# Kernel tuning notes

Measured on AMD Instinct MI355X. Metric: run time of the kernel, lower is better.

The kernel has to match this reference:

```python
import jax, jax.numpy as jnp
import numpy as np

NA_CUTOFF = 30.0
OTHER_CUTOFF = 15.0
THRESHOLDS = jnp.array([0.5, 1.0, 2.0, 4.0], dtype=jnp.float32)


def _cdist(x):
    # x: [b, n, 3] -> [b, n, n] euclidean distances, safe-sqrt (0 grad at 0)
    diff = x[:, :, None, :] - x[:, None, :, :]
    sq = jnp.sum(diff * diff, axis=-1)
    safe = jnp.where(sq > 0, sq, 1.0)
    return jnp.where(sq > 0, jnp.sqrt(safe), 0.0)


def setup_inputs() -> dict:
    key = jax.random.key(0)
    k1, k2, k3, k4, k5 = jax.random.split(key, 5)
    b, n = 2, 4096
    # angstrom-scale coordinates so cutoffs (15/30 A) are meaningful
    true_coords = jax.random.normal(k1, (b, n, 3), dtype=jnp.float32) * 20.0
    pred_coords = true_coords + jax.random.normal(k2, (b, n, 3), dtype=jnp.float32) * 1.0
    is_dna = jax.random.randint(k3, (b, n), 0, 2) > 0
    is_rna = jax.random.randint(k4, (b, n), 0, 2) > 0
    coords_mask = jax.random.randint(k5, (b, n), 0, 2) > 0
    return {
        'pred_coords': pred_coords,
        'true_coords': true_coords,
        'is_dna': is_dna,
        'is_rna': is_rna,
        'coords_mask': coords_mask,
    }


def reference(pred_coords, true_coords, is_dna, is_rna, coords_mask):
    b, n, _ = pred_coords.shape
    pred_dists = _cdist(pred_coords)            # [b, n, n]
    true_dists = _cdist(true_coords)            # [b, n, n]
    dist_diff = jnp.abs(true_dists - pred_dists)
    # eps: sigmoid(threshold - |d_true - d_pred|), averaged over 4 thresholds
    eps = jax.nn.sigmoid(THRESHOLDS - dist_diff[..., None]).mean(axis=-1)  # [b, n, n]

    is_nt = is_dna | is_rna
    nt_pair = is_nt[:, :, None] & is_nt[:, None, :]
    inclusion = jnp.where(nt_pair, true_dists < NA_CUTOFF, true_dists < OTHER_CUTOFF)
    mask = inclusion & ~jnp.eye(n, dtype=bool)[None]
    mask = mask & (coords_mask[:, :, None] & coords_mask[:, None, :])

    maskf = mask.astype(eps.dtype)
    num = (eps * maskf).sum(axis=(-1, -2))
    den = jnp.maximum(maskf.sum(axis=(-1, -2)), 1.0)
    lddt = num / den
    return 1.0 - lddt.mean()
```

## Files before the change

### kernel.cpp

```cpp
#include <hip/hip_runtime.h>
#include <math.h>

#define NTHREADS 256
#define CT4 4

#define LUTN 3072
#define OCT_LO (-16)
#define U_MIN 1.52587890625e-5f
#define U_MAX 255.999f
#define IDX_BYTE_BIAS 56832u

typedef float v2f __attribute__((ext_vector_type(2)));

__device__ __forceinline__ float fsqrt(float x) {
#if __has_builtin(__builtin_amdgcn_sqrtf)
    return __builtin_amdgcn_sqrtf(x);
#else
    return sqrtf(x);
#endif
}
__device__ __forceinline__ float fmed3(float x, float lo, float hi) {
#if __has_builtin(__builtin_amdgcn_fmed3f)
    return __builtin_amdgcn_fmed3f(x, lo, hi);
#else
    return fminf(fmaxf(x, lo), hi);
#endif
}

__device__ __forceinline__ float sig4(float d) {
    const float e = expf(d);
    return 1.0f / (1.0f + e * 0.60653065971263342360f)
         + 1.0f / (1.0f + e * 0.36787944117144232160f)
         + 1.0f / (1.0f + e * 0.13533528323661269189f)
         + 1.0f / (1.0f + e * 0.01831563888873418029f);
}

__global__ __launch_bounds__(256) void lut_build_kernel(float* __restrict__ gLUT) {
    const int e = blockIdx.x * 256 + threadIdx.x;
    if (e < LUTN) {
        const int oct = e >> 7;
        const int k   = e & 127;
        const float base2 = exp2f((float)(oct + OCT_LO));
        const float umid = base2 * (1.0f + ((float)k + 0.5f) * 0.0078125f);
        gLUT[e] = sig4(fsqrt(umid));
    }
}

__device__ __forceinline__ void pair_tail(float sqp, float sqt, float cut2,
                                          const char* __restrict__ lutB,
                                          float& num, float& den) {
    const float r  = fsqrt(sqt * sqp);
    const float u0 = fmaf(-2.0f, r, sqt + sqp);
    const float u  = fmed3(u0, U_MIN, U_MAX);
    const unsigned int bits = __float_as_uint(u);
    const float s  = *(const float*)(lutB + ((bits >> 14) & ~3u));
    const float m  = (sqt < cut2) ? 1.0f : 0.0f;
    num = fmaf(m, s, num);
    den += m;
}

__global__ __launch_bounds__(NTHREADS) void lddt_tile_kernel(
    const float* __restrict__ pred, const float* __restrict__ tru,
    const int* __restrict__ is_dna, const int* __restrict__ is_rna,
    const int* __restrict__ cmask, const float* __restrict__ gLUT,
    float* __restrict__ pnum, float* __restrict__ pden,
    int n, int nsblk)
{
    __shared__ __align__(16) float sPX[256], sPY[256], sPZ[256];
    __shared__ __align__(16) float sTX[256], sTY[256], sTZ[256];
    __shared__ __align__(16) float sCut[2 * 256];
    __shared__ __align__(16) float sLUT[LUTN];
    __shared__ float wnum[4], wden[4];

    const int tid = threadIdx.x;

    int s = blockIdx.x;
    const int bi = s / nsblk;
    s -= bi * nsblk;
    const int q = s >> 2;
    const int r = s & 3;
    const int W = 33;
    int g = (int)(((float)W - fsqrt((float)(W * W - 8 * q))) * 0.5f);
    while ((g + 1) * 16 - ((g + 1) * g) / 2 <= q) ++g;
    while (g * 16 - (g * (g - 1)) / 2 > q) --g;
    const int sc = g + (q - (g * 16 - (g * (g - 1)) / 2));
    const int ti = 4 * g + r;
    const int i0 = 64 * ti;
    const int J0 = 256 * sc;
    const bool has_diag = (sc == g);
    const size_t base = (size_t)bi * n;

    {
        const float4* gl4 = (const float4*)gLUT;
        float4* sl4 = (float4*)sLUT;
        #pragma unroll
        for (int e = tid; e < LUTN / 4; e += NTHREADS) sl4[e] = gl4[e];
    }

    {
        const int j = J0 + tid;
        const float* p = pred + (base + j) * 3;
        const float* qq = tru + (base + j) * 3;
        sPX[tid] = p[0]; sPY[tid] = p[1]; sPZ[tid] = p[2];
        sTX[tid] = qq[0]; sTY[tid] = qq[1]; sTZ[tid] = qq[2];
        const bool ntj = (is_dna[base + j] != 0) || (is_rna[base + j] != 0);
        const bool cmj = (cmask[base + j] != 0);
        sCut[tid]       = cmj ? (ntj ? 900.0f : 225.0f) : 0.0f;
        sCut[256 + tid] = cmj ? 225.0f : 0.0f;
    }

    const int w  = tid >> 6;
    const int l  = tid & 63;
    const int i  = i0 + l;
    const float* p = pred + (base + i) * 3;
    const float* qq = tru + (base + i) * 3;
    const float pix = p[0], piy = p[1], piz = p[2];
    const float tix = qq[0], tiy = qq[1], tiz = qq[2];
    const bool nti = (is_dna[base + i] != 0) || (is_rna[base + i] != 0);
    const float cmf = (cmask[base + i] != 0) ? 1.0f : 0.0f;
    __syncthreads();

    const float* cutsel = nti ? &sCut[0] : &sCut[256];
    const char* lutB = (const char*)sLUT - IDX_BYTE_BIAS;
    const int kbase = 16 * w;

    const v2f px2 = {pix, pix}, py2 = {piy, piy}, pz2 = {piz, piz};
    const v2f tx2 = {tix, tix}, ty2 = {tiy, tiy}, tz2 = {tiz, tiz};

    float accn = 0.0f, accd = 0.0f;

    #pragma unroll
    for (int c = 0; c < CT4; ++c) {
        const int tj = 4 * sc + c;
        if (tj < ti) continue;
        const bool diag = has_diag && (c == r);
        const int o = 64 * c;

        float num = 0.0f, den = 0.0f;
        #pragma unroll
        for (int qd = 0; qd < 4; ++qd) {
            const int jq = o + kbase + 4 * qd;
            const float4 PX = *(const float4*)&sPX[jq];
            const float4 PY = *(const float4*)&sPY[jq];
            const float4 PZ = *(const float4*)&sPZ[jq];
            const float4 TX = *(const float4*)&sTX[jq];
            const float4 TY = *(const float4*)&sTY[jq];
            const float4 TZ = *(const float4*)&sTZ[jq];
            const float4 CTC = *(const float4*)&cutsel[jq];

            v2f dx, dy, dz, sqpA, sqpB, sqtA, sqtB;

            dx = px2 - (v2f){PX.x, PX.y}; dy = py2 - (v2f){PY.x, PY.y}; dz = pz2 - (v2f){PZ.x, PZ.y};
            sqpA = dx * dx + dy * dy + dz * dz;
            dx = tx2 - (v2f){TX.x, TX.y}; dy = ty2 - (v2f){TY.x, TY.y}; dz = tz2 - (v2f){TZ.x, TZ.y};
            sqtA = dx * dx + dy * dy + dz * dz;

            dx = px2 - (v2f){PX.z, PX.w}; dy = py2 - (v2f){PY.z, PY.w}; dz = pz2 - (v2f){PZ.z, PZ.w};
            sqpB = dx * dx + dy * dy + dz * dz;
            dx = tx2 - (v2f){TX.z, TX.w}; dy = ty2 - (v2f){TY.z, TY.w}; dz = tz2 - (v2f){TZ.z, TZ.w};
            sqtB = dx * dx + dy * dy + dz * dz;

            pair_tail(sqpA.x, sqtA.x, CTC.x, lutB, num, den);
            pair_tail(sqpA.y, sqtA.y, CTC.y, lutB, num, den);
            pair_tail(sqpB.x, sqtB.x, CTC.z, lutB, num, den);
            pair_tail(sqpB.y, sqtB.y, CTC.w, lutB, num, den);
        }
        const float sc2 = diag ? 1.0f : 2.0f;
        accn = fmaf(sc2, num, accn);
        accd = fmaf(sc2, den, accd);
    }

    if (has_diag && ((l >> 4) == w)) {
        accn -= sLUT[0];
        accd -= 1.0f;
    }
    accn *= cmf;
    accd *= cmf;

    #pragma unroll
    for (int off = 32; off > 0; off >>= 1) {
        accn += __shfl_down(accn, off, 64);
        accd += __shfl_down(accd, off, 64);
    }
    if ((tid & 63) == 0) { wnum[w] = accn; wden[w] = accd; }
    __syncthreads();

    if (tid == 0) {
        pnum[blockIdx.x] = wnum[0] + wnum[1] + wnum[2] + wnum[3];
        pden[blockIdx.x] = wden[0] + wden[1] + wden[2] + wden[3];
    }
}

__global__ __launch_bounds__(256) void lddt_final_kernel(
    const float* __restrict__ pnum, const float* __restrict__ pden,
    float* __restrict__ out, int nsblk)
{
    __shared__ double sn0[4], sn1[4], sd0[4], sd1[4];
    double n0 = 0, n1 = 0, d0 = 0, d1 = 0;
    for (int s = threadIdx.x; s < 2 * nsblk; s += 256) {
        if (s < nsblk) { n0 += (double)pnum[s]; d0 += (double)pden[s]; }
        else           { n1 += (double)pnum[s]; d1 += (double)pden[s]; }
    }
    #pragma unroll
    for (int off = 32; off > 0; off >>= 1) {
        n0 += __shfl_down(n0, off, 64); d0 += __shfl_down(d0, off, 64);
        n1 += __shfl_down(n1, off, 64); d1 += __shfl_down(d1, off, 64);
    }
    const int w = threadIdx.x >> 6;
    if ((threadIdx.x & 63) == 0) { sn0[w] = n0; sn1[w] = n1; sd0[w] = d0; sd1[w] = d1; }
    __syncthreads();
    if (threadIdx.x == 0) {
        double N0 = sn0[0] + sn0[1] + sn0[2] + sn0[3];
        double N1 = sn1[0] + sn1[1] + sn1[2] + sn1[3];
        double D0 = sd0[0] + sd0[1] + sd0[2] + sd0[3];
        double D1 = sd1[0] + sd1[1] + sd1[2] + sd1[3];
        D0 = D0 > 1.0 ? D0 : 1.0;
        D1 = D1 > 1.0 ? D1 : 1.0;
        const double l0 = 0.25 * N0 / D0;
        const double l1 = 0.25 * N1 / D1;
        out[0] = (float)(1.0 - 0.5 * (l0 + l1));
    }
}

extern "C" void kernel_launch(void* const* d_in, const int* in_sizes, int n_in,
                              void* d_out, int out_size, void* d_ws, size_t ws_size,
                              hipStream_t stream) {
    const float* pred = (const float*)d_in[0];
    const float* tru  = (const float*)d_in[1];
    const int*   dna  = (const int*)d_in[2];
    const int*   rna  = (const int*)d_in[3];
    const int*   cm   = (const int*)d_in[4];
    float* out = (float*)d_out;

    const int B = 2;
    const int n = in_sizes[2] / B;
    const int nsblk = 544;
    (void)n;

    float* gLUT = (float*)d_ws;
    float* pnum = (float*)((char*)d_ws + (size_t)LUTN * sizeof(float));
    float* pden = pnum + (size_t)B * nsblk;

    const int grid = B * nsblk;

    hipLaunchKernelGGL(lut_build_kernel, dim3((LUTN + 255) / 256), dim3(256), 0, stream,
                       gLUT);
    hipLaunchKernelGGL(lddt_tile_kernel, dim3(grid), dim3(NTHREADS), 0, stream,
                       pred, tru, dna, rna, cm, gLUT, pnum, pden, n, nsblk);
    hipLaunchKernelGGL(lddt_final_kernel, dim3(1), dim3(256), 0, stream,
                       pnum, pden, out, nsblk);
}
```

Before: 80.35 us.

## Compact masked atoms before pairwise tiles and skip empty tiles

Adds a pre-pass kernel that stream-compacts atoms with coords_mask set into a padded SoA buffer holding coordinates and cutoff values. The tile kernel then runs over the compacted set and exits early for tiles past the valid count, which removes about three quarters of the pairwise work since roughly half the atoms are masked. The cost is an extra launch and a single-block-per-batch scan with serial per-thread loops. Padding uses far-away coordinates and zero cutoffs so padded pairs contribute nothing.

```diff
diff --git a/kernel.cpp b/kernel.cpp
--- a/kernel.cpp
+++ b/kernel.cpp
@@ -2,7 +2,8 @@
 #include <math.h>
 
 #define NTHREADS 256
-#define CT4 4
+#define CAP 4096
+#define NSBLK 544
 
 #define LUTN 3072
 #define OCT_LO (-16)
@@ -43,6 +44,66 @@
         const float base2 = exp2f((float)(oct + OCT_LO));
         const float umid = base2 * (1.0f + ((float)k + 0.5f) * 0.0078125f);
         gLUT[e] = sig4(fsqrt(umid));
+    }
+}
+
+__global__ __launch_bounds__(256) void compact_kernel(
+    const float* __restrict__ pred, const float* __restrict__ tru,
+    const int* __restrict__ dna, const int* __restrict__ rna,
+    const int* __restrict__ cm,
+    float* __restrict__ C, int* __restrict__ Mout, int n, int S )
+{
+    __shared__ int scan[256];
+    const int b = blockIdx.x;
+    const int tid = threadIdx.x;
+    const size_t base = (size_t)b * n;
+    const int npt = n / 256;
+
+    int cnt = 0;
+    unsigned int flags = 0;
+    for (int k = 0; k < npt; ++k) {
+        const int i = tid * npt + k;
+        const int f = (cm[base + i] != 0) ? 1 : 0;
+        flags |= (unsigned int)f << k;
+        cnt += f;
+    }
+    scan[tid] = cnt;
+    __syncthreads();
+    for (int off = 1; off < 256; off <<= 1) {
+        const int v = scan[tid];
+        const int u = (tid >= off) ? scan[tid - off] : 0;
+        __syncthreads();
+        scan[tid] = v + u;
+        __syncthreads();
+    }
+    const int M = scan[255];
+    int pos = scan[tid] - cnt;
+    if (tid == 0) Mout[b] = M;
+
+    float* cpx = C + 0 * S + b * CAP;  float* cpy = C + 1 * S + b * CAP;
+    float* cpz = C + 2 * S + b * CAP;  float* ctx = C + 3 * S + b * CAP;
+    float* cty = C + 4 * S + b * CAP;  float* ctz = C + 5 * S + b * CAP;
+    float* ccn = C + 6 * S + b * CAP;  float* cco = C + 7 * S + b * CAP;
+    float* cnt_f = C + 8 * S + b * CAP;
+
+    for (int k = 0; k < npt; ++k) {
+        if ((flags >> k) & 1u) {
+            const int i = tid * npt + k;
+            const float* p = pred + (base + i) * 3;
+            const float* q = tru  + (base + i) * 3;
+            const int nt = (dna[base + i] != 0) || (rna[base + i] != 0);
+            cpx[pos] = p[0]; cpy[pos] = p[1]; cpz[pos] = p[2];
+            ctx[pos] = q[0]; cty[pos] = q[1]; ctz[pos] = q[2];
+            ccn[pos] = nt ? 900.0f : 225.0f;
+            cco[pos] = 225.0f;
+            cnt_f[pos] = nt ? 1.0f : 0.0f;
+            ++pos;
+        }
+    }
+    for (int k = M + tid; k < CAP; k += 256) {
+        cpx[k] = 1.0e9f; cpy[k] = 1.0e9f; cpz[k] = 1.0e9f;
+        ctx[k] = 1.0e9f; cty[k] = 1.0e9f; ctz[k] = 1.0e9f;
+        ccn[k] = 0.0f; cco[k] = 0.0f; cnt_f[k] = 0.0f;
     }
 }
 
@@ -60,11 +121,9 @@
 }
 
 __global__ __launch_bounds__(NTHREADS) void lddt_tile_kernel(
-    const float* __restrict__ pred, const float* __restrict__ tru,
-    const int* __restrict__ is_dna, const int* __restrict__ is_rna,
-    const int* __restrict__ cmask, const float* __restrict__ gLUT,
-    float* __restrict__ pnum, float* __restrict__ pden,
-    int n, int nsblk)
+    const float* __restrict__ C, const int* __restrict__ Mptr,
+    const float* __restrict__ gLUT,
+    float* __restrict__ pnum, float* __restrict__ pden, int S)
 {
     __shared__ __align__(16) float sPX[256], sPY[256], sPZ[256];
     __shared__ __align__(16) float sTX[256], sTY[256], sTZ[256];
@@ -75,8 +134,8 @@
     const int tid = threadIdx.x;
 
     int s = blockIdx.x;
-    const int bi = s / nsblk;
-    s -= bi * nsblk;
+    const int bi = s / NSBLK;
+    s -= bi * NSBLK;
     const int q = s >> 2;
     const int r = s & 3;
     const int W = 33;
@@ -88,7 +147,19 @@
     const int i0 = 64 * ti;
     const int J0 = 256 * sc;
     const bool has_diag = (sc == g);
-    const size_t base = (size_t)bi * n;
+    const int M = Mptr[bi];
+
+    if (i0 >= M || J0 >= M) {
+        if (tid == 0) { pnum[blockIdx.x] = 0.0f; pden[blockIdx.x] = 0.0f; }
+        return;
+    }
+
+    const int bo = bi * CAP;
+    const float* cpx = C + 0 * S + bo;  const float* cpy = C + 1 * S + bo;
+    const float* cpz = C + 2 * S + bo;  const float* ctx = C + 3 * S + bo;
+    const float* cty = C + 4 * S + bo;  const float* ctz = C + 5 * S + bo;
+    const float* ccn = C + 6 * S + bo;  const float* cco = C + 7 * S + bo;
+    const float* cntf = C + 8 * S + bo;
 
     {
         const float4* gl4 = (const float4*)gLUT;
@@ -99,25 +170,17 @@
 
     {
         const int j = J0 + tid;
-        const float* p = pred + (base + j) * 3;
-        const float* qq = tru + (base + j) * 3;
-        sPX[tid] = p[0]; sPY[tid] = p[1]; sPZ[tid] = p[2];
-        sTX[tid] = qq[0]; sTY[tid] = qq[1]; sTZ[tid] = qq[2];
-        const bool ntj = (is_dna[base + j] != 0) || (is_rna[base + j] != 0);
-        const bool cmj = (cmask[base + j] != 0);
-        sCut[tid]       = cmj ? (ntj ? 900.0f : 225.0f) : 0.0f;
-        sCut[256 + tid] = cmj ? 225.0f : 0.0f;
-    }
-
-    const int w  = tid >> 6;
-    const int l  = tid & 63;
-    const int i  = i0 + l;
-    const float* p = pred + (base + i) * 3;
-    const float* qq = tru + (base + i) * 3;
-    const float pix = p[0], piy = p[1], piz = p[2];
-    const float tix = qq[0], tiy = qq[1], tiz = qq[2];
-    const bool nti = (is_dna[base + i] != 0) || (is_rna[base + i] != 0);
-    const float cmf = (cmask[base + i] != 0) ? 1.0f : 0.0f;
+        sPX[tid] = cpx[j]; sPY[tid] = cpy[j]; sPZ[tid] = cpz[j];
+        sTX[tid] = ctx[j]; sTY[tid] = cty[j]; sTZ[tid] = ctz[j];
+        sCut[tid] = ccn[j]; sCut[256 + tid] = cco[j];
+    }
+
+    const int w = tid >> 6;
+    const int l = tid & 63;
+    const int i = i0 + l;
+    const float pix = cpx[i], piy = cpy[i], piz = cpz[i];
+    const float tix = ctx[i], tiy = cty[i], tiz = ctz[i];
+    const bool nti = (cntf[i] != 0.0f);
     __syncthreads();
 
     const float* cutsel = nti ? &sCut[0] : &sCut[256];
@@ -130,9 +193,9 @@
     float accn = 0.0f, accd = 0.0f;
 
     #pragma unroll
-    for (int c = 0; c < CT4; ++c) {
+    for (int c = 0; c < 4; ++c) {
         const int tj = 4 * sc + c;
-        if (tj < ti) continue;
+        if (tj < ti || 64 * tj >= M) continue;
         const bool diag = has_diag && (c == r);
         const int o = 64 * c;
 
@@ -170,12 +233,10 @@
         accd = fmaf(sc2, den, accd);
     }
 
-    if (has_diag && ((l >> 4) == w)) {
+    if (has_diag && ((l >> 4) == w) && i < M) {
         accn -= sLUT[0];
         accd -= 1.0f;
     }
-    accn *= cmf;
-    accd *= cmf;
 
     #pragma unroll
     for (int off = 32; off > 0; off >>= 1) {
@@ -234,19 +295,21 @@
 
     const int B = 2;
     const int n = in_sizes[2] / B;
-    const int nsblk = 544;
-    (void)n;
-
-    float* gLUT = (float*)d_ws;
-    float* pnum = (float*)((char*)d_ws + (size_t)LUTN * sizeof(float));
-    float* pden = pnum + (size_t)B * nsblk;
-
-    const int grid = B * nsblk;
+    const int S = B * CAP;
+
+    char* p = (char*)d_ws;
+    float* gLUT = (float*)p;                 p += (size_t)LUTN * sizeof(float);
+    float* C    = (float*)p;                 p += (size_t)9 * S * sizeof(float);
+    float* pnum = (float*)p;                 p += (size_t)B * NSBLK * sizeof(float);
+    float* pden = (float*)p;                 p += (size_t)B * NSBLK * sizeof(float);
+    int*   Mout = (int*)p;
 
     hipLaunchKernelGGL(lut_build_kernel, dim3((LUTN + 255) / 256), dim3(256), 0, stream,
                        gLUT);
-    hipLaunchKernelGGL(lddt_tile_kernel, dim3(grid), dim3(NTHREADS), 0, stream,
-                       pred, tru, dna, rna, cm, gLUT, pnum, pden, n, nsblk);
+    hipLaunchKernelGGL(compact_kernel, dim3(B), dim3(256), 0, stream,
+                       pred, tru, dna, rna, cm, C, Mout, n, S);
+    hipLaunchKernelGGL(lddt_tile_kernel, dim3(B * NSBLK), dim3(NTHREADS), 0, stream,
+                       C, Mout, gLUT, pnum, pden, S);
     hipLaunchKernelGGL(lddt_final_kernel, dim3(1), dim3(256), 0, stream,
-                       pnum, pden, out, nsblk);
-}
+                       pnum, pden, out, NSBLK);
+}
```

After: 93.39 us. 1.16x slower.
